# Performance work log

Measured on AMD Instinct MI355X. Metric: run time of the kernel, lower is better.

## Reference

```python
import jax, jax.numpy as jnp
import numpy as np


def setup_inputs() -> dict:
    key = jax.random.key(0)
    ks = jax.random.split(key, 8)
    B = 65536
    scale = lambda fan_in: 1.0 / np.sqrt(fan_in)
    return {
        "x": jax.random.normal(ks[0], (B, 784), dtype=jnp.float32),
        "w0": jax.random.normal(ks[1], (124, 784), dtype=jnp.float32) * scale(784),
        "w1": jax.random.normal(ks[2], (32, 124), dtype=jnp.float32) * scale(124),
        "w3": jax.random.normal(ks[3], (22, 32), dtype=jnp.float32) * scale(32),
        "b3": jax.random.normal(ks[4], (22,), dtype=jnp.float32) * scale(32),
        "w5": jax.random.normal(ks[5], (21, 22), dtype=jnp.float32) * scale(22),
        "b5": jax.random.normal(ks[6], (21,), dtype=jnp.float32) * scale(22),
        "w7": jax.random.normal(ks[7], (10, 21), dtype=jnp.float32) * scale(21),
    }


def reference(x, w0, w1, w3, b3, w5, b5, w7):
    # x: [B, 784]; PyTorch Linear: y = x @ W.T (+ b)
    h = x @ w0.T                       # [B, 124] (no bias, no activation)
    h = jax.nn.relu(h @ w1.T)          # [B, 32]
    h = jax.nn.relu(h @ w3.T + b3)     # [B, 22]
    h = jax.nn.relu(h @ w5.T + b5)     # [B, 21]
    logits = h @ w7.T                  # [B, 10]
    return jax.nn.log_softmax(logits, axis=1)
```

## Files before the change

### kernel.cpp

```cpp
#include <hip/hip_runtime.h>
#include <hip/hip_fp16.h>

typedef _Float16 half8 __attribute__((ext_vector_type(8)));
typedef __fp16 cvt2_t __attribute__((ext_vector_type(2)));
typedef float f32x4 __attribute__((ext_vector_type(4)));

#define W0F_UNITS (13 * 1024)
#define W1F_OFF   (W0F_UNITS * 16)
#define W1F_UNITS 512
#define SW_OFF    (W1F_OFF + W1F_UNITS * 16)

#define L_XT   0
#define L_H0   8192
#define L_H1   16384
#define L_H3   0
#define L_H5   3200
#define L_OS   6400
#define LDS_SZ 18432

__global__ void prep_weights(const float* __restrict__ w0,
                             const float* __restrict__ w1,
                             const float* __restrict__ w3,
                             const float* __restrict__ b3,
                             const float* __restrict__ w5,
                             const float* __restrict__ b5,
                             const float* __restrict__ w7,
                             char* __restrict__ ws) {
  int tid = blockIdx.x * 256 + threadIdx.x;
  if (tid < W0F_UNITS) {
    int t  = tid >> 10;
    int kf = (tid >> 9) & 1;
    int nf = (tid >> 6) & 7;
    int l  = tid & 63;
    int n  = nf * 16 + (l & 15);
    int k0 = t * 64 + kf * 32 + (l >> 4) * 8;
    alignas(16) __half h[8];
#pragma unroll
    for (int e = 0; e < 8; e++) {
      int k = k0 + e;
      h[e] = __float2half((n < 124 && k < 784) ? w0[n * 784 + k] : 0.f);
    }
    *(uint4*)(ws + tid * 16) = *(const uint4*)h;
    return;
  }
  int r = tid - W0F_UNITS;
  if (r < W1F_UNITS) {
    int kf = r >> 7;
    int nf = (r >> 6) & 1;
    int l  = r & 63;
    int n  = nf * 16 + (l & 15);
    int k0 = kf * 32 + (l >> 4) * 8;
    alignas(16) __half h[8];
#pragma unroll
    for (int e = 0; e < 8; e++) {
      int k = k0 + e;
      h[e] = __float2half((k < 124) ? w1[n * 124 + k] : 0.f);
    }
    *(uint4*)(ws + W1F_OFF + r * 16) = *(const uint4*)h;
    return;
  }
  r -= W1F_UNITS;
  float* sw = (float*)(ws + SW_OFF);
  if (r < 704) { sw[r] = w3[r]; return; }
  r -= 704;
  if (r < 504) {
    int n = r / 24, k = r % 24;
    sw[704 + r] = (k < 22) ? w5[n * 22 + k] : 0.f;
    return;
  }
  r -= 504;
  if (r < 240) {
    int n = r / 24, k = r % 24;
    sw[1208 + r] = (k < 21) ? w7[n * 21 + k] : 0.f;
    return;
  }
  r -= 240;
  if (r < 24) { sw[1448 + r] = (r < 22) ? b3[r] : 0.f; return; }
  r -= 24;
  if (r < 24) { sw[1472 + r] = (r < 21) ? b5[r] : 0.f; return; }
}

__global__ __launch_bounds__(64, 2) void fused_mlp(
    const float* __restrict__ x, const char* __restrict__ ws,
    float* __restrict__ out) {
  __shared__ alignas(16) char sm[LDS_SZ];
  const int l  = threadIdx.x;
  const int lr = l & 15;
  const int lg = l >> 4;
  const size_t row0 = (size_t)blockIdx.x * 32;

  const float* xcol = x + (row0 + lg) * 784 + lr * 4;

  const int wb0 = lg * 128 + ((lr * 8) ^ (lg << 4));
  const int wb1 = wb0 ^ 64;
  const int rb0 = lr * 128 + ((lg * 16) ^ ((lr & 7) << 4));
  const int rb1 = lr * 128 + ((64 + lg * 16) ^ ((lr & 7) << 4));

  f32x4 acc[2][8];
#pragma unroll
  for (int mf = 0; mf < 2; mf++)
#pragma unroll
    for (int nf = 0; nf < 8; nf++) acc[mf][nf] = f32x4{0.f, 0.f, 0.f, 0.f};

  const uint4* wf = (const uint4*)ws;

  f32x4 xr[8];
  half8 bfr[2][8];

#define XLOAD(T, GUARD)                                                        \
  {                                                                            \
    const float* pt = xcol + (size_t)(T) * 64;                                 \
    _Pragma("unroll") for (int i = 0; i < 8; i++) {                            \
      if (!(GUARD) || lr < 4)                                                  \
        xr[i] = __builtin_nontemporal_load((const f32x4*)(pt + i * 3136));     \
      else                                                                     \
        xr[i] = f32x4{0.f, 0.f, 0.f, 0.f};                                     \
    }                                                                          \
  }

#define XSTORE(PAR)                                                            \
  {                                                                            \
    _Pragma("unroll") for (int i = 0; i < 8; i++) {                            \
      cvt2_t q0 = __builtin_amdgcn_cvt_pkrtz(xr[i][0], xr[i][1]);              \
      cvt2_t q1 = __builtin_amdgcn_cvt_pkrtz(xr[i][2], xr[i][3]);              \
      uint2 u;                                                                 \
      u.x = __builtin_bit_cast(unsigned, q0);                                  \
      u.y = __builtin_bit_cast(unsigned, q1);                                  \
      *(uint2*)(sm + L_XT + (PAR) * 4096 + ((i & 1) ? wb1 : wb0) + i * 512) =  \
          u;                                                                   \
    }                                                                          \
  }

#define BFLOAD(T)                                                              \
  _Pragma("unroll") for (int kf = 0; kf < 2; kf++)                             \
      _Pragma("unroll") for (int nf = 0; nf < 8; nf++)                         \
          bfr[kf][nf] = __builtin_bit_cast(                                    \
              half8, wf[(T) * 1024 + kf * 512 + nf * 64 + l]);

  XLOAD(0, false)
  BFLOAD(0)
  XSTORE(0)

#pragma unroll
  for (int T = 0; T < 13; T++) {
    const int par = T & 1;
    if (T < 12) XLOAD(T + 1, (T + 1) == 12)
    {
      half8 af[2][2];
      af[0][0] = *(const half8*)(sm + L_XT + par * 4096 + rb0);
      af[1][0] = *(const half8*)(sm + L_XT + par * 4096 + rb0 + 2048);
      af[0][1] = *(const half8*)(sm + L_XT + par * 4096 + rb1);
      af[1][1] = *(const half8*)(sm + L_XT + par * 4096 + rb1 + 2048);
#pragma unroll
      for (int kf = 0; kf < 2; kf++)
#pragma unroll
        for (int mf = 0; mf < 2; mf++)
#pragma unroll
          for (int nf = 0; nf < 8; nf++)
            acc[mf][nf] = __builtin_amdgcn_mfma_f32_16x16x32_f16(
                af[mf][kf], bfr[kf][nf], acc[mf][nf], 0, 0, 0);
    }
    if (T < 12) {
      BFLOAD(T + 1)
      XSTORE(par ^ 1)
    }
  }

  half8 b1[4][2];
  {
    const uint4* w1f = (const uint4*)(ws + W1F_OFF);
#pragma unroll
    for (int kf = 0; kf < 4; kf++)
#pragma unroll
      for (int nf = 0; nf < 2; nf++)
        b1[kf][nf] = __builtin_bit_cast(half8, w1f[kf * 128 + nf * 64 + l]);
  }

#pragma unroll
  for (int mf = 0; mf < 2; mf++)
#pragma unroll
    for (int nf = 0; nf < 8; nf++)
#pragma unroll
      for (int q = 0; q < 4; q++) {
        int rr = mf * 16 + lg * 4 + q;
        int cc = nf * 16 + lr;
        *(__half*)(sm + L_H0 + rr * 256 + ((2 * cc) ^ ((rr & 7) << 4))) =
            __float2half(acc[mf][nf][q]);
      }
  __syncthreads();

  f32x4 acc1[2][2];
#pragma unroll
  for (int mf = 0; mf < 2; mf++) {
    acc1[mf][0] = f32x4{0.f, 0.f, 0.f, 0.f};
    acc1[mf][1] = f32x4{0.f, 0.f, 0.f, 0.f};
  }
#pragma unroll
  for (int kf = 0; kf < 4; kf++) {
    half8 a1[2];
#pragma unroll
    for (int mf = 0; mf < 2; mf++) {
      int rr = mf * 16 + lr;
      int cb = kf * 64 + lg * 16;
      a1[mf] = *(const half8*)(sm + L_H0 + rr * 256 + (cb ^ ((rr & 7) << 4)));
    }
#pragma unroll
    for (int mf = 0; mf < 2; mf++)
#pragma unroll
      for (int nf = 0; nf < 2; nf++)
        acc1[mf][nf] = __builtin_amdgcn_mfma_f32_16x16x32_f16(
            a1[mf], b1[kf][nf], acc1[mf][nf], 0, 0, 0);
  }
#pragma unroll
  for (int mf = 0; mf < 2; mf++)
#pragma unroll
    for (int nf = 0; nf < 2; nf++)
#pragma unroll
      for (int q = 0; q < 4; q++) {
        int rr = mf * 16 + lg * 4 + q;
        int cc = nf * 16 + lr;
        float v = fmaxf(acc1[mf][nf][q], 0.f);
        *(__half*)(sm + L_H1 + rr * 64 + ((2 * cc) ^ ((rr & 3) << 4))) =
            __float2half(v);
      }
  __syncthreads();

  const int r = l & 31;
  const int j = l >> 5;
  float h1v[32];
#pragma unroll
  for (int cb = 0; cb < 4; cb++) {
    half8 v = *(const half8*)(sm + L_H1 + r * 64 + ((cb * 16) ^ ((r & 3) << 4)));
#pragma unroll
    for (int e = 0; e < 8; e++) h1v[cb * 8 + e] = (float)v[e];
  }
  const float* w3g = (const float*)(ws + SW_OFF);
  const float* w5g = (const float*)(ws + SW_OFF + 2816);
  const float* w7g = (const float*)(ws + SW_OFF + 4832);
  const float* b3g = (const float*)(ws + SW_OFF + 5792);
  const float* b5g = (const float*)(ws + SW_OFF + 5888);
  float* h3l = (float*)(sm + L_H3);
  float* h5l = (float*)(sm + L_H5);

#pragma unroll
  for (int i = 0; i < 11; i++) {
    int n = j + 2 * i;
    float s = b3g[n];
    const float4* wrow = (const float4*)(w3g + n * 32);
#pragma unroll
    for (int kk = 0; kk < 8; kk++) {
      float4 wv = wrow[kk];
      s += h1v[4 * kk] * wv.x + h1v[4 * kk + 1] * wv.y +
           h1v[4 * kk + 2] * wv.z + h1v[4 * kk + 3] * wv.w;
    }
    h3l[r * 25 + n] = fmaxf(s, 0.f);
  }
  __syncthreads();
  float h3v[24];
#pragma unroll
  for (int k = 0; k < 24; k++) h3v[k] = (k < 22) ? h3l[r * 25 + k] : 0.f;
#pragma unroll
  for (int i = 0; i < 11; i++) {
    int n = j + 2 * i;
    if (n < 21) {
      float s = b5g[n];
      const float4* wrow = (const float4*)(w5g + n * 24);
#pragma unroll
      for (int kk = 0; kk < 6; kk++) {
        float4 wv = wrow[kk];
        s += h3v[4 * kk] * wv.x + h3v[4 * kk + 1] * wv.y +
             h3v[4 * kk + 2] * wv.z + h3v[4 * kk + 3] * wv.w;
      }
      h5l[r * 25 + n] = fmaxf(s, 0.f);
    }
  }
  __syncthreads();
  if (j == 0) {
    float h5v[24];
#pragma unroll
    for (int k = 0; k < 24; k++) h5v[k] = (k < 21) ? h5l[r * 25 + k] : 0.f;
    float lgt[10];
    float mx = -3.4e38f;
#pragma unroll
    for (int n = 0; n < 10; n++) {
      float s = 0.f;
      const float4* wrow = (const float4*)(w7g + n * 24);
#pragma unroll
      for (int kk = 0; kk < 6; kk++) {
        float4 wv = wrow[kk];
        s += h5v[4 * kk] * wv.x + h5v[4 * kk + 1] * wv.y +
             h5v[4 * kk + 2] * wv.z + h5v[4 * kk + 3] * wv.w;
      }
      lgt[n] = s;
      mx = fmaxf(mx, s);
    }
    float se = 0.f;
#pragma unroll
    for (int n = 0; n < 10; n++) se += __expf(lgt[n] - mx);
    const float lse = mx + __logf(se);
    float* os = (float*)(sm + L_OS);
#pragma unroll
    for (int n = 0; n < 10; n++) os[r * 10 + n] = lgt[n] - lse;
  }
  __syncthreads();
  {
    const float* os = (const float*)(sm + L_OS);
#pragma unroll
    for (int i = 0; i < 5; i++) out[row0 * 10 + i * 64 + l] = os[i * 64 + l];
  }
}

extern "C" void kernel_launch(void* const* d_in, const int* in_sizes, int n_in,
                              void* d_out, int out_size, void* d_ws, size_t ws_size,
                              hipStream_t stream) {
  const float* x  = (const float*)d_in[0];
  const float* w0 = (const float*)d_in[1];
  const float* w1 = (const float*)d_in[2];
  const float* w3 = (const float*)d_in[3];
  const float* b3 = (const float*)d_in[4];
  const float* w5 = (const float*)d_in[5];
  const float* b5 = (const float*)d_in[6];
  const float* w7 = (const float*)d_in[7];
  float* out = (float*)d_out;
  char* ws = (char*)d_ws;

  const int prep_threads = W0F_UNITS + W1F_UNITS + 704 + 504 + 240 + 24 + 24;
  prep_weights<<<(prep_threads + 255) / 256, 256, 0, stream>>>(w0, w1, w3, b3,
                                                               w5, b5, w7, ws);
  fused_mlp<<<65536 / 32, 64, 0, stream>>>(x, ws, out);
}
```

Baseline: 68.57 us.

## Halve rows per block and deepen K stages to 256 with interleaved weight loads

```diff
diff --git a/kernel.cpp b/kernel.cpp
--- a/kernel.cpp
+++ b/kernel.cpp
@@ -11,12 +11,12 @@
 #define SW_OFF    (W1F_OFF + W1F_UNITS * 16)
 
 #define L_XT   0
-#define L_H0   8192
-#define L_H1   16384
-#define L_H3   0
-#define L_H5   3200
-#define L_OS   6400
-#define LDS_SZ 18432
+#define L_H0   0
+#define L_H1   4096
+#define L_H3   5120
+#define L_H5   6720
+#define L_OS   8320
+#define LDS_SZ 10240
 
 __global__ void prep_weights(const float* __restrict__ w0,
                              const float* __restrict__ w1,
@@ -87,84 +87,104 @@
   const int l  = threadIdx.x;
   const int lr = l & 15;
   const int lg = l >> 4;
-  const size_t row0 = (size_t)blockIdx.x * 32;
-
-  const float* xcol = x + (row0 + lg) * 784 + lr * 4;
-
-  const int wb0 = lg * 128 + ((lr * 8) ^ (lg << 4));
-  const int wb1 = wb0 ^ 64;
-  const int rb0 = lr * 128 + ((lg * 16) ^ ((lr & 7) << 4));
-  const int rb1 = lr * 128 + ((64 + lg * 16) ^ ((lr & 7) << 4));
-
-  f32x4 acc[2][8];
-#pragma unroll
-  for (int mf = 0; mf < 2; mf++)
-#pragma unroll
-    for (int nf = 0; nf < 8; nf++) acc[mf][nf] = f32x4{0.f, 0.f, 0.f, 0.f};
-
+  const size_t row0 = (size_t)blockIdx.x * 16;
   const uint4* wf = (const uint4*)ws;
 
-  f32x4 xr[8];
+  f32x4 acc[8];
+#pragma unroll
+  for (int nf = 0; nf < 8; nf++) acc[nf] = f32x4{0.f, 0.f, 0.f, 0.f};
+
+  f32x4 xg0[8], xg1[8];
   half8 bfr[2][8];
-
-#define XLOAD(T, GUARD)                                                        \
-  {                                                                            \
-    const float* pt = xcol + (size_t)(T) * 64;                                 \
+  half8 af[8];
+
+#define XLOADG(T, XG, RB, GUARD)                                               \
+  {                                                                            \
     _Pragma("unroll") for (int i = 0; i < 8; i++) {                            \
-      if (!(GUARD) || lr < 4)                                                  \
-        xr[i] = __builtin_nontemporal_load((const f32x4*)(pt + i * 3136));     \
-      else                                                                     \
-        xr[i] = f32x4{0.f, 0.f, 0.f, 0.f};                                     \
+      const float* p = x + (row0 + (RB) + i) * 784 + (T) * 256 + 4 * l;        \
+      XG[i] = (!(GUARD) || l < 4) ? *(const f32x4*)p                           \
+                                  : f32x4{0.f, 0.f, 0.f, 0.f};                 \
     }                                                                          \
   }
 
-#define XSTORE(PAR)                                                            \
+#define XSTOREG(XG, RB)                                                        \
   {                                                                            \
     _Pragma("unroll") for (int i = 0; i < 8; i++) {                            \
-      cvt2_t q0 = __builtin_amdgcn_cvt_pkrtz(xr[i][0], xr[i][1]);              \
-      cvt2_t q1 = __builtin_amdgcn_cvt_pkrtz(xr[i][2], xr[i][3]);              \
+      cvt2_t q0 = __builtin_amdgcn_cvt_pkrtz(XG[i][0], XG[i][1]);              \
+      cvt2_t q1 = __builtin_amdgcn_cvt_pkrtz(XG[i][2], XG[i][3]);              \
       uint2 u;                                                                 \
       u.x = __builtin_bit_cast(unsigned, q0);                                  \
       u.y = __builtin_bit_cast(unsigned, q1);                                  \
-      *(uint2*)(sm + L_XT + (PAR) * 4096 + ((i & 1) ? wb1 : wb0) + i * 512) =  \
-          u;                                                                   \
+      *(uint2*)(sm + L_XT + ((RB) + i) * 512 +                                 \
+                ((8 * l) ^ ((((RB) + i) & 7) << 4))) = u;                      \
     }                                                                          \
   }
 
-#define BFLOAD(T)                                                              \
-  _Pragma("unroll") for (int kf = 0; kf < 2; kf++)                             \
-      _Pragma("unroll") for (int nf = 0; nf < 8; nf++)                         \
-          bfr[kf][nf] = __builtin_bit_cast(                                    \
-              half8, wf[(T) * 1024 + kf * 512 + nf * 64 + l]);
-
-  XLOAD(0, false)
-  BFLOAD(0)
-  XSTORE(0)
-
-#pragma unroll
-  for (int T = 0; T < 13; T++) {
-    const int par = T & 1;
-    if (T < 12) XLOAD(T + 1, (T + 1) == 12)
-    {
-      half8 af[2][2];
-      af[0][0] = *(const half8*)(sm + L_XT + par * 4096 + rb0);
-      af[1][0] = *(const half8*)(sm + L_XT + par * 4096 + rb0 + 2048);
-      af[0][1] = *(const half8*)(sm + L_XT + par * 4096 + rb1);
-      af[1][1] = *(const half8*)(sm + L_XT + par * 4096 + rb1 + 2048);
-#pragma unroll
-      for (int kf = 0; kf < 2; kf++)
-#pragma unroll
-        for (int mf = 0; mf < 2; mf++)
-#pragma unroll
-          for (int nf = 0; nf < 8; nf++)
-            acc[mf][nf] = __builtin_amdgcn_mfma_f32_16x16x32_f16(
-                af[mf][kf], bfr[kf][nf], acc[mf][nf], 0, 0, 0);
-    }
-    if (T < 12) {
-      BFLOAD(T + 1)
-      XSTORE(par ^ 1)
-    }
-  }
+#define AREAD1(KF)                                                             \
+  af[KF] = *(const half8*)(sm + L_XT + lr * 512 +                              \
+                           (((KF) * 64 + lg * 16) ^ ((lr & 7) << 4)));
+
+#define AREAD_ALL()                                                            \
+  { _Pragma("unroll") for (int kf = 0; kf < 8; kf++) AREAD1(kf) }
+
+#define BFL(P, G)                                                              \
+  {                                                                            \
+    _Pragma("unroll") for (int nf = 0; nf < 8; nf++)                           \
+      bfr[P][nf] = __builtin_bit_cast(                                         \
+          half8, wf[((G) >> 1) * 1024 + ((G) & 1) * 512 + nf * 64 + l]);       \
+  }
+
+#define MF(KF, P)                                                              \
+  {                                                                            \
+    _Pragma("unroll") for (int nf = 0; nf < 8; nf++)                           \
+      acc[nf] = __builtin_amdgcn_mfma_f32_16x16x32_f16(af[KF], bfr[P][nf],     \
+                                                       acc[nf], 0, 0, 0);      \
+  }
+
+#define BODY(T, STAGE, GUARD)                                                  \
+  {                                                                            \
+    AREAD_ALL()                                                                \
+    BFL(0, (T) * 8 + 0)                                                        \
+    BFL(1, (T) * 8 + 1)                                                        \
+    if (STAGE) {                                                               \
+      XLOADG((T) + 1, xg0, 0, GUARD)                                           \
+      XLOADG((T) + 1, xg1, 8, GUARD)                                           \
+    }                                                                          \
+    MF(0, 0)                                                                   \
+    BFL(0, (T) * 8 + 2)                                                        \
+    MF(1, 1)                                                                   \
+    BFL(1, (T) * 8 + 3)                                                        \
+    MF(2, 0)                                                                   \
+    BFL(0, (T) * 8 + 4)                                                        \
+    MF(3, 1)                                                                   \
+    BFL(1, (T) * 8 + 5)                                                        \
+    MF(4, 0)                                                                   \
+    BFL(0, (T) * 8 + 6)                                                        \
+    MF(5, 1)                                                                   \
+    BFL(1, (T) * 8 + 7)                                                        \
+    MF(6, 0)                                                                   \
+    MF(7, 1)                                                                   \
+    if (STAGE) {                                                               \
+      XSTOREG(xg0, 0)                                                          \
+      XSTOREG(xg1, 8)                                                          \
+    }                                                                          \
+  }
+
+  XLOADG(0, xg0, 0, 0)
+  XLOADG(0, xg1, 8, 0)
+  XSTOREG(xg0, 0)
+  XSTOREG(xg1, 8)
+
+  BODY(0, 1, 0)
+  BODY(1, 1, 0)
+  BODY(2, 1, 1)
+
+  AREAD1(0)
+  AREAD1(1)
+  BFL(0, 24)
+  BFL(1, 25)
+  MF(0, 0)
+  MF(1, 1)
 
   half8 b1[4][2];
   {
@@ -177,56 +197,42 @@
   }
 
 #pragma unroll
-  for (int mf = 0; mf < 2; mf++)
-#pragma unroll
-    for (int nf = 0; nf < 8; nf++)
-#pragma unroll
-      for (int q = 0; q < 4; q++) {
-        int rr = mf * 16 + lg * 4 + q;
-        int cc = nf * 16 + lr;
-        *(__half*)(sm + L_H0 + rr * 256 + ((2 * cc) ^ ((rr & 7) << 4))) =
-            __float2half(acc[mf][nf][q]);
-      }
-  __syncthreads();
-
-  f32x4 acc1[2][2];
-#pragma unroll
-  for (int mf = 0; mf < 2; mf++) {
-    acc1[mf][0] = f32x4{0.f, 0.f, 0.f, 0.f};
-    acc1[mf][1] = f32x4{0.f, 0.f, 0.f, 0.f};
-  }
+  for (int nf = 0; nf < 8; nf++)
+#pragma unroll
+    for (int q = 0; q < 4; q++) {
+      int rr = lg * 4 + q;
+      int cc = nf * 16 + lr;
+      *(__half*)(sm + L_H0 + rr * 256 + ((2 * cc) ^ ((rr & 7) << 4))) =
+          __float2half(acc[nf][q]);
+    }
+  __syncthreads();
+
+  f32x4 acc1[2];
+  acc1[0] = f32x4{0.f, 0.f, 0.f, 0.f};
+  acc1[1] = f32x4{0.f, 0.f, 0.f, 0.f};
 #pragma unroll
   for (int kf = 0; kf < 4; kf++) {
-    half8 a1[2];
-#pragma unroll
-    for (int mf = 0; mf < 2; mf++) {
-      int rr = mf * 16 + lr;
-      int cb = kf * 64 + lg * 16;
-      a1[mf] = *(const half8*)(sm + L_H0 + rr * 256 + (cb ^ ((rr & 7) << 4)));
-    }
-#pragma unroll
-    for (int mf = 0; mf < 2; mf++)
-#pragma unroll
-      for (int nf = 0; nf < 2; nf++)
-        acc1[mf][nf] = __builtin_amdgcn_mfma_f32_16x16x32_f16(
-            a1[mf], b1[kf][nf], acc1[mf][nf], 0, 0, 0);
-  }
-#pragma unroll
-  for (int mf = 0; mf < 2; mf++)
+    int cb = kf * 64 + lg * 16;
+    half8 a1 = *(const half8*)(sm + L_H0 + lr * 256 + (cb ^ ((lr & 7) << 4)));
 #pragma unroll
     for (int nf = 0; nf < 2; nf++)
-#pragma unroll
-      for (int q = 0; q < 4; q++) {
-        int rr = mf * 16 + lg * 4 + q;
-        int cc = nf * 16 + lr;
-        float v = fmaxf(acc1[mf][nf][q], 0.f);
-        *(__half*)(sm + L_H1 + rr * 64 + ((2 * cc) ^ ((rr & 3) << 4))) =
-            __float2half(v);
-      }
-  __syncthreads();
-
-  const int r = l & 31;
-  const int j = l >> 5;
+      acc1[nf] = __builtin_amdgcn_mfma_f32_16x16x32_f16(a1, b1[kf][nf],
+                                                        acc1[nf], 0, 0, 0);
+  }
+#pragma unroll
+  for (int nf = 0; nf < 2; nf++)
+#pragma unroll
+    for (int q = 0; q < 4; q++) {
+      int rr = lg * 4 + q;
+      int cc = nf * 16 + lr;
+      float v = fmaxf(acc1[nf][q], 0.f);
+      *(__half*)(sm + L_H1 + rr * 64 + ((2 * cc) ^ ((rr & 3) << 4))) =
+          __float2half(v);
+    }
+  __syncthreads();
+
+  const int r = l & 15;
+  const int j = l >> 4;
   float h1v[32];
 #pragma unroll
   for (int cb = 0; cb < 4; cb++) {
@@ -243,25 +249,27 @@
   float* h5l = (float*)(sm + L_H5);
 
 #pragma unroll
-  for (int i = 0; i < 11; i++) {
-    int n = j + 2 * i;
-    float s = b3g[n];
-    const float4* wrow = (const float4*)(w3g + n * 32);
-#pragma unroll
-    for (int kk = 0; kk < 8; kk++) {
-      float4 wv = wrow[kk];
-      s += h1v[4 * kk] * wv.x + h1v[4 * kk + 1] * wv.y +
-           h1v[4 * kk + 2] * wv.z + h1v[4 * kk + 3] * wv.w;
-    }
-    h3l[r * 25 + n] = fmaxf(s, 0.f);
+  for (int i = 0; i < 6; i++) {
+    int n = j + 4 * i;
+    if (n < 22) {
+      float s = b3g[n];
+      const float4* wrow = (const float4*)(w3g + n * 32);
+#pragma unroll
+      for (int kk = 0; kk < 8; kk++) {
+        float4 wv = wrow[kk];
+        s += h1v[4 * kk] * wv.x + h1v[4 * kk + 1] * wv.y +
+             h1v[4 * kk + 2] * wv.z + h1v[4 * kk + 3] * wv.w;
+      }
+      h3l[r * 25 + n] = fmaxf(s, 0.f);
+    }
   }
   __syncthreads();
   float h3v[24];
 #pragma unroll
   for (int k = 0; k < 24; k++) h3v[k] = (k < 22) ? h3l[r * 25 + k] : 0.f;
 #pragma unroll
-  for (int i = 0; i < 11; i++) {
-    int n = j + 2 * i;
+  for (int i = 0; i < 6; i++) {
+    int n = j + 4 * i;
     if (n < 21) {
       float s = b5g[n];
       const float4* wrow = (const float4*)(w5g + n * 24);
@@ -305,8 +313,10 @@
   __syncthreads();
   {
     const float* os = (const float*)(sm + L_OS);
-#pragma unroll
-    for (int i = 0; i < 5; i++) out[row0 * 10 + i * 64 + l] = os[i * 64 + l];
+    float* ob = out + (size_t)blockIdx.x * 160;
+    ob[l] = os[l];
+    ob[64 + l] = os[64 + l];
+    if (l < 32) ob[128 + l] = os[128 + l];
   }
 }
 
@@ -327,5 +337,5 @@
   const int prep_threads = W0F_UNITS + W1F_UNITS + 704 + 504 + 240 + 24 + 24;
   prep_weights<<<(prep_threads + 255) / 256, 256, 0, stream>>>(w0, w1, w3, b3,
                                                                w5, b5, w7, ws);
-  fused_mlp<<<65536 / 32, 64, 0, stream>>>(x, ws, out);
+  fused_mlp<<<65536 / 16, 64, 0, stream>>>(x, ws, out);
 }
```

Result: slower. 74.74 us (+9.0%).
